# Kernel optimization log

Hardware: AMD Instinct MI355X
Metric: run time of the kernel (lower is better)

Reference implementation:

```python
import jax, jax.numpy as jnp
import numpy as np

NEG_INF = -1e30


def setup_inputs() -> dict:
    key = jax.random.key(0)
    ks = jax.random.split(key, 6)
    B, S, D, H, DK = 32, 512, 512, 8, 64
    x = jax.random.normal(ks[0], (B, S, D), dtype=jnp.float32)
    mask = jax.random.randint(ks[1], (B, S), 0, 2, dtype=jnp.int32)
    # xavier-uniform-like scale for [D, DK] projections
    lim_qkv = float(np.sqrt(6.0 / (D + DK)))
    lim_o = float(np.sqrt(6.0 / (D + D)))
    Wq = jax.random.uniform(ks[2], (H, D, DK), jnp.float32, -lim_qkv, lim_qkv)
    Wk = jax.random.uniform(ks[3], (H, D, DK), jnp.float32, -lim_qkv, lim_qkv)
    Wv = jax.random.uniform(ks[4], (H, D, DK), jnp.float32, -lim_qkv, lim_qkv)
    Wo = jax.random.uniform(ks[5], (D, D), jnp.float32, -lim_o, lim_o)
    bias = jnp.zeros((1,), dtype=jnp.float32)
    return {"x": x, "mask": mask, "Wq": Wq, "Wk": Wk, "Wv": Wv, "Wo": Wo, "bias": bias}


def reference(x, mask, Wq, Wk, Wv, Wo, bias):
    B, S, D = x.shape
    H, _, DK = Wq.shape
    scale = 1.0 / jnp.sqrt(jnp.float32(DK))
    # Fused per-head QKV projections (original loops over heads)
    Q = jnp.einsum("bsd,hdk->bhsk", x, Wq) + bias  # [B,H,S,DK]
    K = jnp.einsum("bsd,hdk->bhsk", x, Wk) + bias
    V = jnp.einsum("bsd,hdk->bhsk", x, Wv) + bias
    scores = jnp.einsum("bhsk,bhtk->bhst", Q, K) * scale  # [B,H,S,S]
    # CS224N masked_softmax: mask*logits + (1-mask)*(-1e30), softmax over keys
    m = mask.astype(scores.dtype)[:, None, None, :]  # [B,1,1,S]
    masked = m * scores + (1.0 - m) * NEG_INF
    probs = jax.nn.softmax(masked, axis=-1)
    heads = jnp.einsum("bhst,bhtv->bhsv", probs, V)  # [B,H,S,DK]
    multihead = heads.transpose(0, 2, 1, 3).reshape(B, S, H * DK)  # concat heads
    out = jnp.matmul(multihead, Wo) + bias  # [B,S,D]
    return out
```

## Files before the change

### kernel.cpp

```cpp
#include <hip/hip_runtime.h>
#include <hip/hip_bf16.h>
#include <math.h>

#define NB 32
#define NS 512
#define ND 512
#define NH 8
#define NDK 64

typedef __attribute__((ext_vector_type(8))) short bfrag;
typedef __attribute__((ext_vector_type(4))) float f32x4;

#define SCL 0.18033688011112042592f

__device__ __forceinline__ ushort f2bf(float f) {
    union { float f; unsigned u; } v; v.f = f;
    unsigned u = v.u;
    return (ushort)((u + 0x7fffu + ((u >> 16) & 1u)) >> 16);
}

__device__ __forceinline__ unsigned pk2bf(float a, float b) {
    __hip_bfloat162 h = __float22bfloat162_rn(make_float2(a, b));
    return *reinterpret_cast<unsigned*>(&h);
}

__device__ __forceinline__ void async16(const ushort* g, ushort* l) {
    __builtin_amdgcn_global_load_lds(
        (const __attribute__((address_space(1))) unsigned int*)g,
        (__attribute__((address_space(3))) unsigned int*)l, 16, 0, 0);
}

__global__ __launch_bounds__(256) void cvt_x(const float* __restrict__ x,
                                             ushort* __restrict__ xb) {
    const int idx = blockIdx.x * 256 + threadIdx.x;
    const float4 v = reinterpret_cast<const float4*>(x)[idx];
    ushort4 o;
    o.x = f2bf(v.x); o.y = f2bf(v.y); o.z = f2bf(v.z); o.w = f2bf(v.w);
    reinterpret_cast<ushort4*>(xb)[idx] = o;
}

__global__ __launch_bounds__(256) void cvt_w(const float* __restrict__ Wq,
                                             const float* __restrict__ Wk,
                                             const float* __restrict__ Wv,
                                             const float* __restrict__ Wo,
                                             ushort* __restrict__ WT,
                                             ushort* __restrict__ WoT) {
    __shared__ ushort T[64 * 72];
    const int bid = blockIdx.x, tid = threadIdx.x;
    const float* src; ushort* dst; int d0, n0, stride;
    if (bid < 192) {
        const int which = bid >> 6, h = (bid >> 3) & 7, rt = bid & 7;
        const float* Ws = (which == 0) ? Wq : (which == 1) ? Wk : Wv;
        src = Ws + (size_t)h * ND * NDK;
        dst = WT + (size_t)(which * NH + h) * NDK * ND;
        d0 = rt * 64; n0 = 0; stride = NDK;
    } else {
        const int t = bid - 192, rt = t >> 3, ct = t & 7;
        src = Wo; dst = WoT;
        d0 = rt * 64; n0 = ct * 64; stride = ND;
    }
    #pragma unroll
    for (int i = 0; i < 4; i++) {
        const int u = i * 256 + tid;
        const int row = u >> 4, cq = u & 15;
        const float4 v = *reinterpret_cast<const float4*>(&src[(size_t)(d0 + row) * stride + n0 + cq * 4]);
        T[(cq * 4 + 0) * 72 + row] = f2bf(v.x);
        T[(cq * 4 + 1) * 72 + row] = f2bf(v.y);
        T[(cq * 4 + 2) * 72 + row] = f2bf(v.z);
        T[(cq * 4 + 3) * 72 + row] = f2bf(v.w);
    }
    __syncthreads();
    #pragma unroll
    for (int i = 0; i < 2; i++) {
        const int u = i * 256 + tid;
        const int n = u >> 3, dq = u & 7;
        *reinterpret_cast<float4*>(&dst[(size_t)(n0 + n) * ND + d0 + dq * 8]) =
            *reinterpret_cast<float4*>(&T[n * 72 + dq * 8]);
    }
}

__global__ __launch_bounds__(256) void qk_gemm(const ushort* __restrict__ xb,
                                               const ushort* __restrict__ WT,
                                               const float* __restrict__ bias,
                                               ushort* __restrict__ QKb) {
    __shared__ ushort As[128 * 64];
    __shared__ ushort Bs[128 * 64];
    const int bid = blockIdx.x;
    const int m0 = (bid & 127) * 128, n0 = (bid >> 7) * 128;
    const int tid = threadIdx.x;
    const int w = tid >> 6, lane = tid & 63, quad = lane >> 4, l16 = lane & 15;
    const int lr = lane >> 3, lc = lane & 7, cs = lc ^ lr, swz = l16 & 7;
    const int rw = (w & 1) * 64, cw = (w >> 1) * 64;

    f32x4 acc[4][4];
    #pragma unroll
    for (int i = 0; i < 4; i++)
        #pragma unroll
        for (int j = 0; j < 4; j++) acc[i][j] = (f32x4){0.f, 0.f, 0.f, 0.f};

    for (int d0 = 0; d0 < ND; d0 += 64) {
        __syncthreads();
        #pragma unroll
        for (int t = 0; t < 4; t++) {
            const int rb = (w * 4 + t) * 8;
            async16(&xb[(size_t)(m0 + rb + lr) * ND + d0 + cs * 8], &As[rb * 64]);
            const int slot = rb + lr, nn = slot & 63;
            const int j = n0 + (slot & 64) + 4 * (nn & 15) + (nn >> 4);
            async16(&WT[(size_t)j * ND + d0 + cs * 8], &Bs[rb * 64]);
        }
        __syncthreads();
        #pragma unroll
        for (int ks = 0; ks < 2; ks++) {
            const int ch = ((ks * 4 + quad) ^ swz) * 8;
            bfrag a[4], bo[4];
            #pragma unroll
            for (int rf = 0; rf < 4; rf++) a[rf] = *(const bfrag*)&As[(rw + rf * 16 + l16) * 64 + ch];
            #pragma unroll
            for (int cf = 0; cf < 4; cf++) bo[cf] = *(const bfrag*)&Bs[(cw + cf * 16 + l16) * 64 + ch];
            #pragma unroll
            for (int rf = 0; rf < 4; rf++)
                #pragma unroll
                for (int cf = 0; cf < 4; cf++)
                    acc[rf][cf] = __builtin_amdgcn_mfma_f32_16x16x32_bf16(a[rf], bo[cf], acc[rf][cf], 0, 0, 0);
        }
    }

    const float bb = bias[0];
    #pragma unroll
    for (int rf = 0; rf < 4; rf++)
        #pragma unroll
        for (int r = 0; r < 4; r++) {
            const int row = m0 + rw + rf * 16 + quad * 4 + r;
            uint2 u;
            u.x = pk2bf(acc[rf][0][r] + bb, acc[rf][1][r] + bb);
            u.y = pk2bf(acc[rf][2][r] + bb, acc[rf][3][r] + bb);
            *(uint2*)&QKb[(size_t)row * 1024 + n0 + cw + 4 * l16] = u;
        }
}

__global__ __launch_bounds__(256) void vt_gemm(const ushort* __restrict__ xb,
                                               const ushort* __restrict__ WT,
                                               const float* __restrict__ bias,
                                               ushort* __restrict__ VT) {
    __shared__ ushort As[64 * 64];
    __shared__ ushort Bs[256 * 64];
    const int bid = blockIdx.x;
    const int bh = bid >> 1, s0 = (bid & 1) * 256;
    const int b = bh >> 3, h = bh & 7;
    const int tid = threadIdx.x;
    const int w = tid >> 6, lane = tid & 63, quad = lane >> 4, l16 = lane & 15;
    const int lr = lane >> 3, lc = lane & 7, cs = lc ^ lr, swz = l16 & 7;
    const int cw = w * 64;

    const ushort* Av = WT + (size_t)(2 * NH + h) * NDK * ND;
    const ushort* xrow = xb + (size_t)b * NS * ND;

    f32x4 acc[4][4];
    #pragma unroll
    for (int i = 0; i < 4; i++)
        #pragma unroll
        for (int j = 0; j < 4; j++) acc[i][j] = (f32x4){0.f, 0.f, 0.f, 0.f};

    for (int d0 = 0; d0 < ND; d0 += 64) {
        __syncthreads();
        #pragma unroll
        for (int t = 0; t < 2; t++) {
            const int rb = w * 16 + t * 8;
            async16(&Av[(size_t)(rb + lr) * ND + d0 + cs * 8], &As[rb * 64]);
        }
        #pragma unroll
        for (int t = 0; t < 8; t++) {
            const int rb = (w * 8 + t) * 8;
            const int slot = rb + lr, nn = slot & 63;
            const int js = s0 + (slot & 192) + 4 * (nn & 15) + (nn >> 4);
            async16(&xrow[(size_t)js * ND + d0 + cs * 8], &Bs[rb * 64]);
        }
        __syncthreads();
        #pragma unroll
        for (int ks = 0; ks < 2; ks++) {
            const int ch = ((ks * 4 + quad) ^ swz) * 8;
            bfrag a[4], bo[4];
            #pragma unroll
            for (int rf = 0; rf < 4; rf++) a[rf] = *(const bfrag*)&As[(rf * 16 + l16) * 64 + ch];
            #pragma unroll
            for (int cf = 0; cf < 4; cf++) bo[cf] = *(const bfrag*)&Bs[(cw + cf * 16 + l16) * 64 + ch];
            #pragma unroll
            for (int rf = 0; rf < 4; rf++)
                #pragma unroll
                for (int cf = 0; cf < 4; cf++)
                    acc[rf][cf] = __builtin_amdgcn_mfma_f32_16x16x32_bf16(a[rf], bo[cf], acc[rf][cf], 0, 0, 0);
        }
    }

    const float bb = bias[0];
    ushort* vbase = VT + (size_t)bh * NDK * NS;
    #pragma unroll
    for (int rf = 0; rf < 4; rf++)
        #pragma unroll
        for (int r = 0; r < 4; r++) {
            const int dk = rf * 16 + quad * 4 + r;
            uint2 u;
            u.x = pk2bf(acc[rf][0][r] + bb, acc[rf][1][r] + bb);
            u.y = pk2bf(acc[rf][2][r] + bb, acc[rf][3][r] + bb);
            *(uint2*)&vbase[(size_t)dk * NS + s0 + cw + 4 * l16] = u;
        }
}

__global__ __launch_bounds__(256) void attn_mfma(const ushort* __restrict__ QKb,
                                                 const ushort* __restrict__ VT,
                                                 const int* __restrict__ mask,
                                                 ushort* __restrict__ Hb) {
    __shared__ ushort Qs[64 * 64];
    __shared__ ushort Ks[64 * 64];
    __shared__ ushort Vs[64 * 64];
    __shared__ ushort Ps[64 * 72];
    const int id = blockIdx.x;
    const int b = id >> 6, h = (id >> 3) & 7, s0 = (id & 7) * 64;
    const int tid = threadIdx.x;
    const int wave = tid >> 6, lane = tid & 63, quad = lane >> 4, l16 = lane & 15;
    const int lr = lane >> 3, lc = lane & 7, cs = lc ^ lr, swz = l16 & 7;

    const ushort* qbase = QKb + (size_t)(b * NS + s0) * 1024 + h * 64;
    const ushort* kbase = QKb + (size_t)(b * NS) * 1024 + 512 + h * 64;
    const ushort* vbase = VT + (size_t)(b * NH + h) * NDK * NS;

    #pragma unroll
    for (int t = 0; t < 2; t++) {
        const int rb = (wave * 2 + t) * 8;
        async16(&qbase[(size_t)(rb + lr) * 1024 + cs * 8], &Qs[rb * 64]);
    }

    bfrag ones;
    #pragma unroll
    for (int i = 0; i < 8; i++) ones[i] = (short)0x3F80;

    f32x4 acc_l = (f32x4){0.f, 0.f, 0.f, 0.f};
    f32x4 acc_o[4];
    #pragma unroll
    for (int c = 0; c < 4; c++) acc_o[c] = (f32x4){0.f, 0.f, 0.f, 0.f};

    for (int kt = 0; kt < 8; kt++) {
        __syncthreads();
        #pragma unroll
        for (int t = 0; t < 2; t++) {
            const int rb = (wave * 2 + t) * 8;
            const int n = rb + lr;
            const int jk = 4 * (n & 15) + (n >> 4);
            async16(&kbase[(size_t)(kt * 64 + jk) * 1024 + cs * 8], &Ks[rb * 64]);
            async16(&vbase[(size_t)jk * NS + kt * 64 + cs * 8], &Vs[rb * 64]);
        }
        __syncthreads();

        f32x4 sc[4];
        #pragma unroll
        for (int c = 0; c < 4; c++) sc[c] = (f32x4){0.f, 0.f, 0.f, 0.f};
        #pragma unroll
        for (int ks = 0; ks < 2; ks++) {
            const int ch = ((ks * 4 + quad) ^ swz) * 8;
            const bfrag a = *(const bfrag*)&Qs[(wave * 16 + l16) * 64 + ch];
            #pragma unroll
            for (int c = 0; c < 4; c++) {
                const bfrag bo = *(const bfrag*)&Ks[(c * 16 + l16) * 64 + ch];
                sc[c] = __builtin_amdgcn_mfma_f32_16x16x32_bf16(a, bo, sc[c], 0, 0, 0);
            }
        }

        const int4 mk4 = *(const int4*)&mask[b * NS + kt * 64 + 4 * l16];
        const int mks[4] = {mk4.x, mk4.y, mk4.z, mk4.w};
        #pragma unroll
        for (int c = 0; c < 4; c++) {
            float p[4];
            #pragma unroll
            for (int r = 0; r < 4; r++)
                p[r] = exp2f(mks[c] ? sc[c][r] * SCL : -INFINITY);
            sc[c][0] = p[0]; sc[c][1] = p[1]; sc[c][2] = p[2]; sc[c][3] = p[3];
        }
        #pragma unroll
        for (int r = 0; r < 4; r++) {
            uint2 u;
            u.x = pk2bf(sc[0][r], sc[1][r]);
            u.y = pk2bf(sc[2][r], sc[3][r]);
            *(uint2*)&Ps[(wave * 16 + quad * 4 + r) * 72 + l16 * 4] = u;
        }

        #pragma unroll
        for (int ks = 0; ks < 2; ks++) {
            const bfrag a = *(const bfrag*)&Ps[(wave * 16 + l16) * 72 + ks * 32 + quad * 8];
            acc_l = __builtin_amdgcn_mfma_f32_16x16x32_bf16(a, ones, acc_l, 0, 0, 0);
            const int ch = ((ks * 4 + quad) ^ swz) * 8;
            #pragma unroll
            for (int c = 0; c < 4; c++) {
                const bfrag bo = *(const bfrag*)&Vs[(c * 16 + l16) * 64 + ch];
                acc_o[c] = __builtin_amdgcn_mfma_f32_16x16x32_bf16(a, bo, acc_o[c], 0, 0, 0);
            }
        }
    }

    ushort* hbase = Hb + (size_t)(b * NS + s0) * ND + h * 64;
    #pragma unroll
    for (int r = 0; r < 4; r++) {
        const float inv = 1.0f / acc_l[r];
        const int row = wave * 16 + quad * 4 + r;
        uint2 u;
        u.x = pk2bf(acc_o[0][r] * inv, acc_o[1][r] * inv);
        u.y = pk2bf(acc_o[2][r] * inv, acc_o[3][r] * inv);
        *(uint2*)&hbase[(size_t)row * ND + 4 * l16] = u;
    }
}

__global__ __launch_bounds__(256) void out_gemm(const ushort* __restrict__ Hb,
                                                const ushort* __restrict__ WoT,
                                                const float* __restrict__ bias,
                                                float* __restrict__ out) {
    __shared__ ushort As[128 * 64];
    __shared__ ushort Bs[128 * 64];
    const int bid = blockIdx.x;
    const int m0 = (bid & 127) * 128, n0 = (bid >> 7) * 128;
    const int tid = threadIdx.x;
    const int w = tid >> 6, lane = tid & 63, quad = lane >> 4, l16 = lane & 15;
    const int lr = lane >> 3, lc = lane & 7, cs = lc ^ lr, swz = l16 & 7;
    const int rw = (w & 1) * 64, cw = (w >> 1) * 64;

    f32x4 acc[4][4];
    #pragma unroll
    for (int i = 0; i < 4; i++)
        #pragma unroll
        for (int j = 0; j < 4; j++) acc[i][j] = (f32x4){0.f, 0.f, 0.f, 0.f};

    for (int d0 = 0; d0 < ND; d0 += 64) {
        __syncthreads();
        #pragma unroll
        for (int t = 0; t < 4; t++) {
            const int rb = (w * 4 + t) * 8;
            async16(&Hb[(size_t)(m0 + rb + lr) * ND + d0 + cs * 8], &As[rb * 64]);
            const int slot = rb + lr, nn = slot & 63;
            const int j = n0 + (slot & 64) + 4 * (nn & 15) + (nn >> 4);
            async16(&WoT[(size_t)j * ND + d0 + cs * 8], &Bs[rb * 64]);
        }
        __syncthreads();
        #pragma unroll
        for (int ks = 0; ks < 2; ks++) {
            const int ch = ((ks * 4 + quad) ^ swz) * 8;
            bfrag a[4], bo[4];
            #pragma unroll
            for (int rf = 0; rf < 4; rf++) a[rf] = *(const bfrag*)&As[(rw + rf * 16 + l16) * 64 + ch];
            #pragma unroll
            for (int cf = 0; cf < 4; cf++) bo[cf] = *(const bfrag*)&Bs[(cw + cf * 16 + l16) * 64 + ch];
            #pragma unroll
            for (int rf = 0; rf < 4; rf++)
                #pragma unroll
                for (int cf = 0; cf < 4; cf++)
                    acc[rf][cf] = __builtin_amdgcn_mfma_f32_16x16x32_bf16(a[rf], bo[cf], acc[rf][cf], 0, 0, 0);
        }
    }

    const float bb = bias[0];
    #pragma unroll
    for (int rf = 0; rf < 4; rf++)
        #pragma unroll
        for (int r = 0; r < 4; r++) {
            const int row = m0 + rw + rf * 16 + quad * 4 + r;
            float4 v;
            v.x = acc[rf][0][r] + bb; v.y = acc[rf][1][r] + bb;
            v.z = acc[rf][2][r] + bb; v.w = acc[rf][3][r] + bb;
            *(float4*)&out[(size_t)row * ND + n0 + cw + 4 * l16] = v;
        }
}

extern "C" void kernel_launch(void* const* d_in, const int* in_sizes, int n_in,
                              void* d_out, int out_size, void* d_ws, size_t ws_size,
                              hipStream_t stream) {
    const float* x    = (const float*)d_in[0];
    const int*   mask = (const int*)  d_in[1];
    const float* Wq   = (const float*)d_in[2];
    const float* Wk   = (const float*)d_in[3];
    const float* Wv   = (const float*)d_in[4];
    const float* Wo   = (const float*)d_in[5];
    const float* bias = (const float*)d_in[6];
    float* out = (float*)d_out;

    const size_t TE = (size_t)NB * NS * ND;
    ushort* xb  = (ushort*)d_ws;
    ushort* WT  = xb  + TE;
    ushort* WoT = WT  + (size_t)3 * NH * NDK * ND;
    ushort* QKb = WoT + (size_t)ND * ND;
    ushort* VT  = QKb + (size_t)NB * NS * 2 * ND;
    ushort* Hb  = VT  + TE;

    cvt_x<<<dim3((NB * NS * ND) / 1024), dim3(256), 0, stream>>>(x, xb);
    cvt_w<<<dim3(256), dim3(256), 0, stream>>>(Wq, Wk, Wv, Wo, WT, WoT);
    qk_gemm<<<dim3(1024), dim3(256), 0, stream>>>(xb, WT, bias, QKb);
    vt_gemm<<<dim3(512), dim3(256), 0, stream>>>(xb, WT, bias, VT);
    attn_mfma<<<dim3(NB * NH * (NS / 64)), dim3(256), 0, stream>>>(
        QKb, VT, mask, Hb);
    out_gemm<<<dim3(512), dim3(256), 0, stream>>>(Hb, WoT, bias, out);
}
```

Measured before the change: 198.5 us.

## Merge conversion and projection launches, enlarge attention query tile to 128 rows

The x and weight conversion kernels are merged into one launch, and the QK and V projection GEMMs are merged into one launch that branches on block index. Separately, the attention kernel now processes 128 query rows per block with two row fragments per wave, so each K/V tile loaded into shared memory is reused by twice as many queries. The grid is also reordered so blocks sharing a batch-head are spread out. This cuts launch overhead and K/V reload traffic, at the cost of more registers, more shared memory per attention block and half as many attention blocks.

Result: faster. 188.4 us (-5.1%).

```diff
diff --git a/kernel.cpp b/kernel.cpp
--- a/kernel.cpp
+++ b/kernel.cpp
@@ -30,23 +30,25 @@
         (__attribute__((address_space(3))) unsigned int*)l, 16, 0, 0);
 }
 
-__global__ __launch_bounds__(256) void cvt_x(const float* __restrict__ x,
-                                             ushort* __restrict__ xb) {
-    const int idx = blockIdx.x * 256 + threadIdx.x;
-    const float4 v = reinterpret_cast<const float4*>(x)[idx];
-    ushort4 o;
-    o.x = f2bf(v.x); o.y = f2bf(v.y); o.z = f2bf(v.z); o.w = f2bf(v.w);
-    reinterpret_cast<ushort4*>(xb)[idx] = o;
-}
-
-__global__ __launch_bounds__(256) void cvt_w(const float* __restrict__ Wq,
-                                             const float* __restrict__ Wk,
-                                             const float* __restrict__ Wv,
-                                             const float* __restrict__ Wo,
-                                             ushort* __restrict__ WT,
-                                             ushort* __restrict__ WoT) {
+__global__ __launch_bounds__(256) void prep(const float* __restrict__ x,
+                                            const float* __restrict__ Wq,
+                                            const float* __restrict__ Wk,
+                                            const float* __restrict__ Wv,
+                                            const float* __restrict__ Wo,
+                                            ushort* __restrict__ xb,
+                                            ushort* __restrict__ WT,
+                                            ushort* __restrict__ WoT) {
     __shared__ ushort T[64 * 72];
-    const int bid = blockIdx.x, tid = threadIdx.x;
+    const int tid = threadIdx.x;
+    if (blockIdx.x < 8192) {
+        const int idx = blockIdx.x * 256 + tid;
+        const float4 v = reinterpret_cast<const float4*>(x)[idx];
+        ushort4 o;
+        o.x = f2bf(v.x); o.y = f2bf(v.y); o.z = f2bf(v.z); o.w = f2bf(v.w);
+        reinterpret_cast<ushort4*>(xb)[idx] = o;
+        return;
+    }
+    const int bid = blockIdx.x - 8192;
     const float* src; ushort* dst; int d0, n0, stride;
     if (bid < 192) {
         const int which = bid >> 6, h = (bid >> 3) & 7, rt = bid & 7;
@@ -79,18 +81,16 @@
     }
 }
 
-__global__ __launch_bounds__(256) void qk_gemm(const ushort* __restrict__ xb,
-                                               const ushort* __restrict__ WT,
-                                               const float* __restrict__ bias,
-                                               ushort* __restrict__ QKb) {
-    __shared__ ushort As[128 * 64];
-    __shared__ ushort Bs[128 * 64];
-    const int bid = blockIdx.x;
-    const int m0 = (bid & 127) * 128, n0 = (bid >> 7) * 128;
+__global__ __launch_bounds__(256) void proj(const ushort* __restrict__ xb,
+                                            const ushort* __restrict__ WT,
+                                            const float* __restrict__ bias,
+                                            ushort* __restrict__ QKb,
+                                            ushort* __restrict__ VT) {
+    __shared__ ushort sm[20480];
     const int tid = threadIdx.x;
     const int w = tid >> 6, lane = tid & 63, quad = lane >> 4, l16 = lane & 15;
     const int lr = lane >> 3, lc = lane & 7, cs = lc ^ lr, swz = l16 & 7;
-    const int rw = (w & 1) * 64, cw = (w >> 1) * 64;
+    const float bb = bias[0];
 
     f32x4 acc[4][4];
     #pragma unroll
@@ -98,126 +98,114 @@
         #pragma unroll
         for (int j = 0; j < 4; j++) acc[i][j] = (f32x4){0.f, 0.f, 0.f, 0.f};
 
-    for (int d0 = 0; d0 < ND; d0 += 64) {
-        __syncthreads();
-        #pragma unroll
-        for (int t = 0; t < 4; t++) {
-            const int rb = (w * 4 + t) * 8;
-            async16(&xb[(size_t)(m0 + rb + lr) * ND + d0 + cs * 8], &As[rb * 64]);
-            const int slot = rb + lr, nn = slot & 63;
-            const int j = n0 + (slot & 64) + 4 * (nn & 15) + (nn >> 4);
-            async16(&WT[(size_t)j * ND + d0 + cs * 8], &Bs[rb * 64]);
-        }
-        __syncthreads();
-        #pragma unroll
-        for (int ks = 0; ks < 2; ks++) {
-            const int ch = ((ks * 4 + quad) ^ swz) * 8;
-            bfrag a[4], bo[4];
-            #pragma unroll
-            for (int rf = 0; rf < 4; rf++) a[rf] = *(const bfrag*)&As[(rw + rf * 16 + l16) * 64 + ch];
-            #pragma unroll
-            for (int cf = 0; cf < 4; cf++) bo[cf] = *(const bfrag*)&Bs[(cw + cf * 16 + l16) * 64 + ch];
-            #pragma unroll
-            for (int rf = 0; rf < 4; rf++)
-                #pragma unroll
-                for (int cf = 0; cf < 4; cf++)
-                    acc[rf][cf] = __builtin_amdgcn_mfma_f32_16x16x32_bf16(a[rf], bo[cf], acc[rf][cf], 0, 0, 0);
-        }
-    }
-
-    const float bb = bias[0];
-    #pragma unroll
-    for (int rf = 0; rf < 4; rf++)
-        #pragma unroll
-        for (int r = 0; r < 4; r++) {
-            const int row = m0 + rw + rf * 16 + quad * 4 + r;
-            uint2 u;
-            u.x = pk2bf(acc[rf][0][r] + bb, acc[rf][1][r] + bb);
-            u.y = pk2bf(acc[rf][2][r] + bb, acc[rf][3][r] + bb);
-            *(uint2*)&QKb[(size_t)row * 1024 + n0 + cw + 4 * l16] = u;
-        }
-}
-
-__global__ __launch_bounds__(256) void vt_gemm(const ushort* __restrict__ xb,
-                                               const ushort* __restrict__ WT,
-                                               const float* __restrict__ bias,
-                                               ushort* __restrict__ VT) {
-    __shared__ ushort As[64 * 64];
-    __shared__ ushort Bs[256 * 64];
-    const int bid = blockIdx.x;
-    const int bh = bid >> 1, s0 = (bid & 1) * 256;
-    const int b = bh >> 3, h = bh & 7;
-    const int tid = threadIdx.x;
-    const int w = tid >> 6, lane = tid & 63, quad = lane >> 4, l16 = lane & 15;
-    const int lr = lane >> 3, lc = lane & 7, cs = lc ^ lr, swz = l16 & 7;
-    const int cw = w * 64;
-
-    const ushort* Av = WT + (size_t)(2 * NH + h) * NDK * ND;
-    const ushort* xrow = xb + (size_t)b * NS * ND;
-
-    f32x4 acc[4][4];
-    #pragma unroll
-    for (int i = 0; i < 4; i++)
-        #pragma unroll
-        for (int j = 0; j < 4; j++) acc[i][j] = (f32x4){0.f, 0.f, 0.f, 0.f};
-
-    for (int d0 = 0; d0 < ND; d0 += 64) {
-        __syncthreads();
-        #pragma unroll
-        for (int t = 0; t < 2; t++) {
-            const int rb = w * 16 + t * 8;
-            async16(&Av[(size_t)(rb + lr) * ND + d0 + cs * 8], &As[rb * 64]);
-        }
-        #pragma unroll
-        for (int t = 0; t < 8; t++) {
-            const int rb = (w * 8 + t) * 8;
-            const int slot = rb + lr, nn = slot & 63;
-            const int js = s0 + (slot & 192) + 4 * (nn & 15) + (nn >> 4);
-            async16(&xrow[(size_t)js * ND + d0 + cs * 8], &Bs[rb * 64]);
-        }
-        __syncthreads();
-        #pragma unroll
-        for (int ks = 0; ks < 2; ks++) {
-            const int ch = ((ks * 4 + quad) ^ swz) * 8;
-            bfrag a[4], bo[4];
-            #pragma unroll
-            for (int rf = 0; rf < 4; rf++) a[rf] = *(const bfrag*)&As[(rf * 16 + l16) * 64 + ch];
-            #pragma unroll
-            for (int cf = 0; cf < 4; cf++) bo[cf] = *(const bfrag*)&Bs[(cw + cf * 16 + l16) * 64 + ch];
-            #pragma unroll
-            for (int rf = 0; rf < 4; rf++)
-                #pragma unroll
-                for (int cf = 0; cf < 4; cf++)
-                    acc[rf][cf] = __builtin_amdgcn_mfma_f32_16x16x32_bf16(a[rf], bo[cf], acc[rf][cf], 0, 0, 0);
-        }
-    }
-
-    const float bb = bias[0];
-    ushort* vbase = VT + (size_t)bh * NDK * NS;
-    #pragma unroll
-    for (int rf = 0; rf < 4; rf++)
-        #pragma unroll
-        for (int r = 0; r < 4; r++) {
-            const int dk = rf * 16 + quad * 4 + r;
-            uint2 u;
-            u.x = pk2bf(acc[rf][0][r] + bb, acc[rf][1][r] + bb);
-            u.y = pk2bf(acc[rf][2][r] + bb, acc[rf][3][r] + bb);
-            *(uint2*)&vbase[(size_t)dk * NS + s0 + cw + 4 * l16] = u;
-        }
+    if (blockIdx.x < 1024) {
+        ushort* As = sm;
+        ushort* Bs = sm + 8192;
+        const int bid = blockIdx.x;
+        const int m0 = (bid & 127) * 128, n0 = (bid >> 7) * 128;
+        const int rw = (w & 1) * 64, cw = (w >> 1) * 64;
+        for (int d0 = 0; d0 < ND; d0 += 64) {
+            __syncthreads();
+            #pragma unroll
+            for (int t = 0; t < 4; t++) {
+                const int rb = (w * 4 + t) * 8;
+                async16(&xb[(size_t)(m0 + rb + lr) * ND + d0 + cs * 8], &As[rb * 64]);
+                const int slot = rb + lr, nn = slot & 63;
+                const int j = n0 + (slot & 64) + 4 * (nn & 15) + (nn >> 4);
+                async16(&WT[(size_t)j * ND + d0 + cs * 8], &Bs[rb * 64]);
+            }
+            __syncthreads();
+            #pragma unroll
+            for (int ks = 0; ks < 2; ks++) {
+                const int ch = ((ks * 4 + quad) ^ swz) * 8;
+                bfrag a[4], bo[4];
+                #pragma unroll
+                for (int rf = 0; rf < 4; rf++) a[rf] = *(const bfrag*)&As[(rw + rf * 16 + l16) * 64 + ch];
+                #pragma unroll
+                for (int cf = 0; cf < 4; cf++) bo[cf] = *(const bfrag*)&Bs[(cw + cf * 16 + l16) * 64 + ch];
+                #pragma unroll
+                for (int rf = 0; rf < 4; rf++)
+                    #pragma unroll
+                    for (int cf = 0; cf < 4; cf++)
+                        acc[rf][cf] = __builtin_amdgcn_mfma_f32_16x16x32_bf16(a[rf], bo[cf], acc[rf][cf], 0, 0, 0);
+            }
+        }
+        #pragma unroll
+        for (int rf = 0; rf < 4; rf++)
+            #pragma unroll
+            for (int r = 0; r < 4; r++) {
+                const int row = m0 + rw + rf * 16 + quad * 4 + r;
+                uint2 u;
+                u.x = pk2bf(acc[rf][0][r] + bb, acc[rf][1][r] + bb);
+                u.y = pk2bf(acc[rf][2][r] + bb, acc[rf][3][r] + bb);
+                *(uint2*)&QKb[(size_t)row * 1024 + n0 + cw + 4 * l16] = u;
+            }
+    } else {
+        ushort* As = sm;
+        ushort* Bs = sm + 4096;
+        const int bid = blockIdx.x - 1024;
+        const int bh = bid >> 1, s0 = (bid & 1) * 256;
+        const int b = bh >> 3, h = bh & 7;
+        const int cw = w * 64;
+        const ushort* Av = WT + (size_t)(2 * NH + h) * NDK * ND;
+        const ushort* xrow = xb + (size_t)b * NS * ND;
+        for (int d0 = 0; d0 < ND; d0 += 64) {
+            __syncthreads();
+            #pragma unroll
+            for (int t = 0; t < 2; t++) {
+                const int rb = w * 16 + t * 8;
+                async16(&Av[(size_t)(rb + lr) * ND + d0 + cs * 8], &As[rb * 64]);
+            }
+            #pragma unroll
+            for (int t = 0; t < 8; t++) {
+                const int rb = (w * 8 + t) * 8;
+                const int slot = rb + lr, nn = slot & 63;
+                const int js = s0 + (slot & 192) + 4 * (nn & 15) + (nn >> 4);
+                async16(&xrow[(size_t)js * ND + d0 + cs * 8], &Bs[rb * 64]);
+            }
+            __syncthreads();
+            #pragma unroll
+            for (int ks = 0; ks < 2; ks++) {
+                const int ch = ((ks * 4 + quad) ^ swz) * 8;
+                bfrag a[4], bo[4];
+                #pragma unroll
+                for (int rf = 0; rf < 4; rf++) a[rf] = *(const bfrag*)&As[(rf * 16 + l16) * 64 + ch];
+                #pragma unroll
+                for (int cf = 0; cf < 4; cf++) bo[cf] = *(const bfrag*)&Bs[(cw + cf * 16 + l16) * 64 + ch];
+                #pragma unroll
+                for (int rf = 0; rf < 4; rf++)
+                    #pragma unroll
+                    for (int cf = 0; cf < 4; cf++)
+                        acc[rf][cf] = __builtin_amdgcn_mfma_f32_16x16x32_bf16(a[rf], bo[cf], acc[rf][cf], 0, 0, 0);
+            }
+        }
+        ushort* vbase = VT + (size_t)bh * NDK * NS;
+        #pragma unroll
+        for (int rf = 0; rf < 4; rf++)
+            #pragma unroll
+            for (int r = 0; r < 4; r++) {
+                const int dk = rf * 16 + quad * 4 + r;
+                uint2 u;
+                u.x = pk2bf(acc[rf][0][r] + bb, acc[rf][1][r] + bb);
+                u.y = pk2bf(acc[rf][2][r] + bb, acc[rf][3][r] + bb);
+                *(uint2*)&vbase[(size_t)dk * NS + s0 + cw + 4 * l16] = u;
+            }
+    }
 }
 
 __global__ __launch_bounds__(256) void attn_mfma(const ushort* __restrict__ QKb,
                                                  const ushort* __restrict__ VT,
                                                  const int* __restrict__ mask,
                                                  ushort* __restrict__ Hb) {
-    __shared__ ushort Qs[64 * 64];
+    __shared__ ushort Qs[128 * 64];
     __shared__ ushort Ks[64 * 64];
     __shared__ ushort Vs[64 * 64];
-    __shared__ ushort Ps[64 * 72];
+    __shared__ ushort Ps[128 * 72];
     const int id = blockIdx.x;
-    const int b = id >> 6, h = (id >> 3) & 7, s0 = (id & 7) * 64;
+    const int bh = id & 255, b = bh >> 3, h = bh & 7;
+    const int s0 = (id >> 8) * 128;
     const int tid = threadIdx.x;
-    const int wave = tid >> 6, lane = tid & 63, quad = lane >> 4, l16 = lane & 15;
+    const int w = tid >> 6, lane = tid & 63, quad = lane >> 4, l16 = lane & 15;
     const int lr = lane >> 3, lc = lane & 7, cs = lc ^ lr, swz = l16 & 7;
 
     const ushort* qbase = QKb + (size_t)(b * NS + s0) * 1024 + h * 64;
@@ -225,8 +213,8 @@
     const ushort* vbase = VT + (size_t)(b * NH + h) * NDK * NS;
 
     #pragma unroll
-    for (int t = 0; t < 2; t++) {
-        const int rb = (wave * 2 + t) * 8;
+    for (int t = 0; t < 4; t++) {
+        const int rb = (w * 4 + t) * 8;
         async16(&qbase[(size_t)(rb + lr) * 1024 + cs * 8], &Qs[rb * 64]);
     }
 
@@ -234,16 +222,20 @@
     #pragma unroll
     for (int i = 0; i < 8; i++) ones[i] = (short)0x3F80;
 
-    f32x4 acc_l = (f32x4){0.f, 0.f, 0.f, 0.f};
-    f32x4 acc_o[4];
-    #pragma unroll
-    for (int c = 0; c < 4; c++) acc_o[c] = (f32x4){0.f, 0.f, 0.f, 0.f};
+    f32x4 acc_l[2];
+    f32x4 acc_o[2][4];
+    #pragma unroll
+    for (int rf = 0; rf < 2; rf++) {
+        acc_l[rf] = (f32x4){0.f, 0.f, 0.f, 0.f};
+        #pragma unroll
+        for (int c = 0; c < 4; c++) acc_o[rf][c] = (f32x4){0.f, 0.f, 0.f, 0.f};
+    }
 
     for (int kt = 0; kt < 8; kt++) {
         __syncthreads();
         #pragma unroll
         for (int t = 0; t < 2; t++) {
-            const int rb = (wave * 2 + t) * 8;
+            const int rb = (w * 2 + t) * 8;
             const int n = rb + lr;
             const int jk = 4 * (n & 15) + (n >> 4);
             async16(&kbase[(size_t)(kt * 64 + jk) * 1024 + cs * 8], &Ks[rb * 64]);
@@ -251,61 +243,73 @@
         }
         __syncthreads();
 
-        f32x4 sc[4];
-        #pragma unroll
-        for (int c = 0; c < 4; c++) sc[c] = (f32x4){0.f, 0.f, 0.f, 0.f};
+        f32x4 sc[2][4];
+        #pragma unroll
+        for (int rf = 0; rf < 2; rf++)
+            #pragma unroll
+            for (int c = 0; c < 4; c++) sc[rf][c] = (f32x4){0.f, 0.f, 0.f, 0.f};
         #pragma unroll
         for (int ks = 0; ks < 2; ks++) {
             const int ch = ((ks * 4 + quad) ^ swz) * 8;
-            const bfrag a = *(const bfrag*)&Qs[(wave * 16 + l16) * 64 + ch];
-            #pragma unroll
-            for (int c = 0; c < 4; c++) {
-                const bfrag bo = *(const bfrag*)&Ks[(c * 16 + l16) * 64 + ch];
-                sc[c] = __builtin_amdgcn_mfma_f32_16x16x32_bf16(a, bo, sc[c], 0, 0, 0);
-            }
+            bfrag a[2], bo[4];
+            #pragma unroll
+            for (int rf = 0; rf < 2; rf++) a[rf] = *(const bfrag*)&Qs[(w * 32 + rf * 16 + l16) * 64 + ch];
+            #pragma unroll
+            for (int c = 0; c < 4; c++) bo[c] = *(const bfrag*)&Ks[(c * 16 + l16) * 64 + ch];
+            #pragma unroll
+            for (int rf = 0; rf < 2; rf++)
+                #pragma unroll
+                for (int c = 0; c < 4; c++)
+                    sc[rf][c] = __builtin_amdgcn_mfma_f32_16x16x32_bf16(a[rf], bo[c], sc[rf][c], 0, 0, 0);
         }
 
         const int4 mk4 = *(const int4*)&mask[b * NS + kt * 64 + 4 * l16];
         const int mks[4] = {mk4.x, mk4.y, mk4.z, mk4.w};
         #pragma unroll
-        for (int c = 0; c < 4; c++) {
-            float p[4];
-            #pragma unroll
-            for (int r = 0; r < 4; r++)
-                p[r] = exp2f(mks[c] ? sc[c][r] * SCL : -INFINITY);
-            sc[c][0] = p[0]; sc[c][1] = p[1]; sc[c][2] = p[2]; sc[c][3] = p[3];
-        }
+        for (int rf = 0; rf < 2; rf++) {
+            #pragma unroll
+            for (int c = 0; c < 4; c++)
+                #pragma unroll
+                for (int r = 0; r < 4; r++)
+                    sc[rf][c][r] = exp2f(mks[c] ? sc[rf][c][r] * SCL : -INFINITY);
+            #pragma unroll
+            for (int r = 0; r < 4; r++) {
+                uint2 u;
+                u.x = pk2bf(sc[rf][0][r], sc[rf][1][r]);
+                u.y = pk2bf(sc[rf][2][r], sc[rf][3][r]);
+                *(uint2*)&Ps[(w * 32 + rf * 16 + quad * 4 + r) * 72 + l16 * 4] = u;
+            }
+        }
+
+        #pragma unroll
+        for (int ks = 0; ks < 2; ks++) {
+            const int ch = ((ks * 4 + quad) ^ swz) * 8;
+            bfrag bo[4];
+            #pragma unroll
+            for (int c = 0; c < 4; c++) bo[c] = *(const bfrag*)&Vs[(c * 16 + l16) * 64 + ch];
+            #pragma unroll
+            for (int rf = 0; rf < 2; rf++) {
+                const bfrag a = *(const bfrag*)&Ps[(w * 32 + rf * 16 + l16) * 72 + ks * 32 + quad * 8];
+                acc_l[rf] = __builtin_amdgcn_mfma_f32_16x16x32_bf16(a, ones, acc_l[rf], 0, 0, 0);
+                #pragma unroll
+                for (int c = 0; c < 4; c++)
+                    acc_o[rf][c] = __builtin_amdgcn_mfma_f32_16x16x32_bf16(a, bo[c], acc_o[rf][c], 0, 0, 0);
+            }
+        }
+    }
+
+    ushort* hbase = Hb + (size_t)(b * NS + s0) * ND + h * 64;
+    #pragma unroll
+    for (int rf = 0; rf < 2; rf++)
         #pragma unroll
         for (int r = 0; r < 4; r++) {
+            const float inv = 1.0f / acc_l[rf][r];
+            const int row = w * 32 + rf * 16 + quad * 4 + r;
             uint2 u;
-            u.x = pk2bf(sc[0][r], sc[1][r]);
-            u.y = pk2bf(sc[2][r], sc[3][r]);
-            *(uint2*)&Ps[(wave * 16 + quad * 4 + r) * 72 + l16 * 4] = u;
-        }
-
-        #pragma unroll
-        for (int ks = 0; ks < 2; ks++) {
-            const bfrag a = *(const bfrag*)&Ps[(wave * 16 + l16) * 72 + ks * 32 + quad * 8];
-            acc_l = __builtin_amdgcn_mfma_f32_16x16x32_bf16(a, ones, acc_l, 0, 0, 0);
-            const int ch = ((ks * 4 + quad) ^ swz) * 8;
-            #pragma unroll
-            for (int c = 0; c < 4; c++) {
-                const bfrag bo = *(const bfrag*)&Vs[(c * 16 + l16) * 64 + ch];
-                acc_o[c] = __builtin_amdgcn_mfma_f32_16x16x32_bf16(a, bo, acc_o[c], 0, 0, 0);
-            }
-        }
-    }
-
-    ushort* hbase = Hb + (size_t)(b * NS + s0) * ND + h * 64;
-    #pragma unroll
-    for (int r = 0; r < 4; r++) {
-        const float inv = 1.0f / acc_l[r];
-        const int row = wave * 16 + quad * 4 + r;
-        uint2 u;
-        u.x = pk2bf(acc_o[0][r] * inv, acc_o[1][r] * inv);
-        u.y = pk2bf(acc_o[2][r] * inv, acc_o[3][r] * inv);
-        *(uint2*)&hbase[(size_t)row * ND + 4 * l16] = u;
-    }
+            u.x = pk2bf(acc_o[rf][0][r] * inv, acc_o[rf][1][r] * inv);
+            u.y = pk2bf(acc_o[rf][2][r] * inv, acc_o[rf][3][r] * inv);
+            *(uint2*)&hbase[(size_t)row * ND + 4 * l16] = u;
+        }
 }
 
 __global__ __launch_bounds__(256) void out_gemm(const ushort* __restrict__ Hb,
@@ -387,11 +391,8 @@
     ushort* VT  = QKb + (size_t)NB * NS * 2 * ND;
     ushort* Hb  = VT  + TE;
 
-    cvt_x<<<dim3((NB * NS * ND) / 1024), dim3(256), 0, stream>>>(x, xb);
-    cvt_w<<<dim3(256), dim3(256), 0, stream>>>(Wq, Wk, Wv, Wo, WT, WoT);
-    qk_gemm<<<dim3(1024), dim3(256), 0, stream>>>(xb, WT, bias, QKb);
-    vt_gemm<<<dim3(512), dim3(256), 0, stream>>>(xb, WT, bias, VT);
-    attn_mfma<<<dim3(NB * NH * (NS / 64)), dim3(256), 0, stream>>>(
-        QKb, VT, mask, Hb);
+    prep<<<dim3(8448), dim3(256), 0, stream>>>(x, Wq, Wk, Wv, Wo, xb, WT, WoT);
+    proj<<<dim3(1536), dim3(256), 0, stream>>>(xb, WT, bias, QKb, VT);
+    attn_mfma<<<dim3(1024), dim3(256), 0, stream>>>(QKb, VT, mask, Hb);
     out_gemm<<<dim3(512), dim3(256), 0, stream>>>(Hb, WoT, bias, out);
 }
```
